# Kernel optimization log

Measured on AMD Instinct MI355X. Metric: run time of the kernel, lower is better.

The kernel has to match this reference:

```python
import jax, jax.numpy as jnp
import numpy as np

N = 100_000      # nodes
E = 1_600_000    # nonzeros of the rescaled Laplacian (avg degree 16)
F_IN = 128
F_OUT = 128
K = 4


def setup_inputs() -> dict:
    key = jax.random.key(0)
    ks = jax.random.split(key, 6)
    x = jax.random.normal(ks[0], (N, F_IN), dtype=jnp.float32)
    filter_coeff = jax.random.normal(ks[1], (K, N), dtype=jnp.float32)
    # glorot-ish scale for [K, F_in, F_out]
    stdv = float(np.sqrt(6.0 / (F_IN + F_OUT)))
    weight = jax.random.uniform(ks[2], (K, F_IN, F_OUT), dtype=jnp.float32,
                                minval=-stdv, maxval=stdv)
    bias = jnp.zeros((F_OUT,), dtype=jnp.float32)
    src = jax.random.randint(ks[3], (E,), 0, N, dtype=jnp.int32)
    dst = jax.random.randint(ks[4], (E,), 0, N, dtype=jnp.int32)
    # edge values of L_hat = 2L/lambda_max - I (precomputed sparse matrix)
    edge_w = jax.random.normal(ks[5], (E,), dtype=jnp.float32) * 0.1
    return {"x": x, "filter_coeff": filter_coeff, "weight": weight,
            "bias": bias, "edge_w": edge_w, "src": src, "dst": dst}


def reference(x, filter_coeff, weight, bias, edge_w, src, dst):
    n = x.shape[0]

    def spmm(h):  # edge-weighted gather-scale-segment_sum == dgl.update_all
        return jax.ops.segment_sum(h[src] * edge_w[:, None], dst,
                                   num_segments=n)

    # Chebyshev recurrence: T0 = x, T1 = L_hat x, T_k = 2 L_hat T_{k-1} - T_{k-2}
    Tx0 = x
    out = (filter_coeff[0][:, None] * Tx0) @ weight[0]
    Tx1 = spmm(x)
    out = out + (filter_coeff[1][:, None] * Tx1) @ weight[1]
    for k in range(2, weight.shape[0]):
        Tx2 = 2.0 * spmm(Tx1) - Tx0
        out = out + (filter_coeff[k][:, None] * Tx2) @ weight[k]
        Tx0, Tx1 = Tx1, Tx2
    return out + bias
```

## Files before the change

kernel.cpp:

```cpp
#include <hip/hip_runtime.h>
#include <hip/hip_bf16.h>
#include <cstdio>

#define F 128
#define BSHIFT 9
#define BROWS 512
#define C2 4096

typedef __attribute__((ext_vector_type(4))) float f32x4;
typedef __attribute__((ext_vector_type(4))) unsigned short u16x4;
typedef __attribute__((ext_vector_type(8))) short s16x8;

__device__ inline unsigned short f2bf(float x) {
  unsigned int u = __float_as_uint(x);
  u += 0x7fffu + ((u >> 16) & 1u);
  return (unsigned short)(u >> 16);
}
__device__ inline float bf2f(unsigned int h) {
  return __uint_as_float(h << 16);
}

__device__ inline void async_load16(const void* g, void* l) {
  __builtin_amdgcn_global_load_lds(
      (const __attribute__((address_space(1))) void*)g,
      (__attribute__((address_space(3))) void*)l, 16, 0, 0);
}

__global__ void bucket_hist_kernel(const int* __restrict__ dst, int* __restrict__ bhist,
                                   int E, int B) {
  __shared__ int h[256];
  int t = threadIdx.x;
  h[t] = 0;
  __syncthreads();
  for (int e = blockIdx.x * blockDim.x + t; e < E; e += gridDim.x * blockDim.x)
    atomicAdd(&h[dst[e] >> BSHIFT], 1);
  __syncthreads();
  if (t < B && h[t]) atomicAdd(&bhist[t], h[t]);
}

__global__ void bucket_scan_kernel(const int* __restrict__ bhist, int* __restrict__ bbase,
                                   int* __restrict__ bcursor, int* __restrict__ rp,
                                   int E, int B, int N) {
  __shared__ int sm[256];
  int t = threadIdx.x;
  int v = (t < B) ? bhist[t] : 0;
  sm[t] = v;
  __syncthreads();
  int x = v;
  for (int off = 1; off < 256; off <<= 1) {
    int add = (t >= off) ? sm[t - off] : 0;
    __syncthreads();
    x += add;
    sm[t] = x;
    __syncthreads();
  }
  int excl = x - v;
  if (t < B) { bbase[t] = excl; bcursor[t] = excl; }
  if (t == 0) { bbase[B] = E; rp[N] = E; }
}

__global__ __launch_bounds__(256) void bucket_scatter_kernel(
    const int* __restrict__ src, const int* __restrict__ dst, const float* __restrict__ ew,
    int* __restrict__ bcursor, unsigned int* __restrict__ stg_p, float* __restrict__ stg_w,
    int E, int B) {
  __shared__ int hist[256], gbase[256], cur[256], sm[256], scn[256];
  __shared__ unsigned int sp[C2];
  __shared__ float swt[C2];
  __shared__ int sdest[C2];
  int t = threadIdx.x;
  int e0 = blockIdx.x * C2;
  int cnt = min(C2, E - e0);
  hist[t] = 0;
  __syncthreads();
#pragma unroll
  for (int i = 0; i < C2 / 256; ++i) {
    int e = e0 + t + i * 256;
    if (e < E) atomicAdd(&hist[dst[e] >> BSHIFT], 1);
  }
  __syncthreads();
  int v = hist[t];
  gbase[t] = (t < B && v) ? atomicAdd(&bcursor[t], v) : 0;
  sm[t] = v;
  __syncthreads();
  int x = v;
  for (int off = 1; off < 256; off <<= 1) {
    int add = (t >= off) ? sm[t - off] : 0;
    __syncthreads();
    x += add;
    sm[t] = x;
    __syncthreads();
  }
  scn[t] = x - v;
  cur[t] = 0;
  __syncthreads();
#pragma unroll
  for (int i = 0; i < C2 / 256; ++i) {
    int e = e0 + t + i * 256;
    if (e < E) {
      int d = dst[e];
      int b = d >> BSHIFT;
      int r = atomicAdd(&cur[b], 1);
      int slot = scn[b] + r;
      sp[slot] = (unsigned int)src[e] | ((unsigned int)(d & (BROWS - 1)) << 17);
      swt[slot] = ew[e];
      sdest[slot] = gbase[b] + r;
    }
  }
  __syncthreads();
#pragma unroll
  for (int i = 0; i < C2 / 256; ++i) {
    int s = t + i * 256;
    if (s < cnt) {
      int dpos = sdest[s];
      stg_p[dpos] = sp[s];
      stg_w[dpos] = swt[s];
    }
  }
}

__global__ __launch_bounds__(256) void csr_build_kernel(
    const unsigned int* __restrict__ stg_p, const float* __restrict__ stg_w,
    const int* __restrict__ bbase, int* __restrict__ rp, int2* __restrict__ csr,
    int N, int B) {
  __shared__ int rhist[BROWS], rloc[BROWS], curp[BROWS];
  __shared__ int sm[256];
  int b = blockIdx.x, t = threadIdx.x;
  int row0 = b << BSHIFT;
  int base = bbase[b];
  int cnt = bbase[b + 1] - base;
  rhist[t] = 0;
  rhist[t + 256] = 0;
  __syncthreads();
  for (int s = base + t; s < base + cnt; s += 256)
    atomicAdd(&rhist[stg_p[s] >> 17], 1);
  __syncthreads();
  int a0 = rhist[2 * t], a1 = rhist[2 * t + 1];
  int pv = a0 + a1;
  sm[t] = pv;
  __syncthreads();
  int x = pv;
  for (int off = 1; off < 256; off <<= 1) {
    int add = (t >= off) ? sm[t - off] : 0;
    __syncthreads();
    x += add;
    sm[t] = x;
    __syncthreads();
  }
  int pexcl = x - pv;
  int r0 = 2 * t, r1 = 2 * t + 1;
  rloc[r0] = pexcl;
  rloc[r1] = pexcl + a0;
  if (row0 + r0 < N) rp[row0 + r0] = base + rloc[r0];
  if (row0 + r1 < N) rp[row0 + r1] = base + rloc[r1];
  curp[r0] = base + rloc[r0];
  curp[r1] = base + rloc[r1];
  __syncthreads();
  for (int s = base + t; s < base + cnt; s += 256) {
    unsigned int p = stg_p[s];
    int dl = p >> 17;
    int pos = atomicAdd(&curp[dl], 1);
    int2 entry;
    entry.x = (int)(p & 0x1ffffu);
    entry.y = __float_as_int(stg_w[s]);
    csr[pos] = entry;
  }
}

__global__ void convx_kernel(const float* __restrict__ x, unsigned short* __restrict__ xbf,
                             int total4) {
  int i = blockIdx.x * 256 + threadIdx.x;
  if (i >= total4) return;
  f32x4 v = ((const f32x4*)x)[i];
  u16x4 o;
  o.x = f2bf(v.x); o.y = f2bf(v.y); o.z = f2bf(v.z); o.w = f2bf(v.w);
  ((u16x4*)xbf)[i] = o;
}

__global__ __launch_bounds__(256) void spmm_kernel(
    const unsigned short* __restrict__ Tin, const unsigned short* __restrict__ Tsub,
    unsigned short* __restrict__ Tout, const int* __restrict__ rp,
    const int2* __restrict__ csr, int n, float scale) {
  int row = blockIdx.x * 16 + (threadIdx.x >> 4);
  if (row >= n) return;
  int sl = threadIdx.x & 15;
  int j0 = rp[row], end = rp[row + 1];
  const uint4* Tin4 = (const uint4*)Tin;
  float acc[8];
#pragma unroll
  for (int c = 0; c < 8; ++c) acc[c] = 0.f;

  for (int j = j0; j < end; j += 8) {
    int2 e[8];
#pragma unroll
    for (int u = 0; u < 8; ++u)
      if (j + u < end) e[u] = csr[j + u];
    uint4 v[8];
#pragma unroll
    for (int u = 0; u < 8; ++u)
      if (j + u < end) v[u] = Tin4[(size_t)e[u].x * 16 + sl];
#pragma unroll
    for (int u = 0; u < 8; ++u) {
      if (j + u < end) {
        float w = __int_as_float(e[u].y);
        acc[0] = fmaf(w, bf2f(v[u].x & 0xffffu), acc[0]);
        acc[1] = fmaf(w, bf2f(v[u].x >> 16), acc[1]);
        acc[2] = fmaf(w, bf2f(v[u].y & 0xffffu), acc[2]);
        acc[3] = fmaf(w, bf2f(v[u].y >> 16), acc[3]);
        acc[4] = fmaf(w, bf2f(v[u].z & 0xffffu), acc[4]);
        acc[5] = fmaf(w, bf2f(v[u].z >> 16), acc[5]);
        acc[6] = fmaf(w, bf2f(v[u].w & 0xffffu), acc[6]);
        acc[7] = fmaf(w, bf2f(v[u].w >> 16), acc[7]);
      }
    }
  }

  float r[8];
#pragma unroll
  for (int c = 0; c < 8; ++c) r[c] = scale * acc[c];
  if (Tsub) {
    uint4 p = ((const uint4*)Tsub)[(size_t)row * 16 + sl];
    r[0] -= bf2f(p.x & 0xffffu); r[1] -= bf2f(p.x >> 16);
    r[2] -= bf2f(p.y & 0xffffu); r[3] -= bf2f(p.y >> 16);
    r[4] -= bf2f(p.z & 0xffffu); r[5] -= bf2f(p.z >> 16);
    r[6] -= bf2f(p.w & 0xffffu); r[7] -= bf2f(p.w >> 16);
  }
  uint4 o;
  o.x = (unsigned)f2bf(r[0]) | ((unsigned)f2bf(r[1]) << 16);
  o.y = (unsigned)f2bf(r[2]) | ((unsigned)f2bf(r[3]) << 16);
  o.z = (unsigned)f2bf(r[4]) | ((unsigned)f2bf(r[5]) << 16);
  o.w = (unsigned)f2bf(r[6]) | ((unsigned)f2bf(r[7]) << 16);
  ((uint4*)Tout)[(size_t)row * 16 + sl] = o;
}

__global__ void convw_kernel(const float* __restrict__ W, unsigned short* __restrict__ Wf,
                             int total) {
  int idx = blockIdx.x * 256 + threadIdx.x;
  if (idx >= total) return;
  int j = idx & 7;
  int lane = (idx >> 3) & 63;
  int nt = (idx >> 9) & 7;
  int kk = (idx >> 12) & 3;
  int ks = idx >> 14;
  int kl = kk * 32 + (lane >> 4) * 8 + j;
  int col = nt * 16 + (lane & 15);
  Wf[idx] = f2bf(W[(size_t)ks * F * F + (size_t)kl * F + col]);
}

struct GemmArgs {
  const unsigned short* A[8];
  const float* fc;
  const unsigned short* Wt;
  const float* bias;
  float* out;
  int n;
  int kslices;
};

__global__ __launch_bounds__(512) void gemm_kernel(GemmArgs args) {
  __shared__ __align__(16) unsigned short SA[16384];
  __shared__ __align__(16) unsigned short SB[16384];
  const int t = threadIdx.x;
  const int lane = t & 63;
  const int wid = t >> 6;
  const int wrow = wid >> 1;
  const int wcol = wid & 1;
  const int n = args.n;
  const int bm = blockIdx.x * 128;
  const int arow = lane & 15;
  const int kg = lane >> 4;

  f32x4 Cf[2][4];
#pragma unroll
  for (int mt = 0; mt < 2; ++mt)
#pragma unroll
    for (int nt = 0; nt < 4; ++nt) Cf[mt][nt] = (f32x4){0.f, 0.f, 0.f, 0.f};

  for (int ks = 0; ks < args.kslices; ++ks) {
    const unsigned short* As = args.A[ks];
#pragma unroll
    for (int i = 0; i < 4; ++i) {
      int fi = wid + i * 8;
      int rg = fi >> 2, kk = fi & 3;
      int r = bm + rg * 16 + arow;
      if (r >= n) r = n - 1;
      const void* g = (const void*)(As + (size_t)r * F + kk * 32 + kg * 8);
      async_load16(g, (void*)(SA + fi * 512));
    }
#pragma unroll
    for (int i = 0; i < 4; ++i) {
      int fi = wid + i * 8;
      const void* g = (const void*)(args.Wt + (size_t)ks * 16384 + fi * 512 + lane * 8);
      async_load16(g, (void*)(SB + fi * 512));
    }
    __syncthreads();

    f32x4 acc[2][4];
#pragma unroll
    for (int mt = 0; mt < 2; ++mt)
#pragma unroll
      for (int nt = 0; nt < 4; ++nt) acc[mt][nt] = (f32x4){0.f, 0.f, 0.f, 0.f};

#pragma unroll
    for (int kk = 0; kk < 4; ++kk) {
      s16x8 af[2], bfr[4];
#pragma unroll
      for (int mt = 0; mt < 2; ++mt) {
        int rg = wrow * 2 + mt;
        af[mt] = *(const s16x8*)&SA[(rg * 4 + kk) * 512 + lane * 8];
      }
#pragma unroll
      for (int nt = 0; nt < 4; ++nt)
        bfr[nt] = *(const s16x8*)&SB[(kk * 8 + wcol * 4 + nt) * 512 + lane * 8];
#pragma unroll
      for (int mt = 0; mt < 2; ++mt)
#pragma unroll
        for (int nt = 0; nt < 4; ++nt)
          acc[mt][nt] = __builtin_amdgcn_mfma_f32_16x16x32_bf16(af[mt], bfr[nt],
                                                                acc[mt][nt], 0, 0, 0);
    }

#pragma unroll
    for (int mt = 0; mt < 2; ++mt) {
      int row = bm + wrow * 32 + mt * 16 + kg * 4;
      f32x4 fv;
      if (row + 3 < n) {
        fv = *(const f32x4*)(args.fc + (size_t)ks * n + row);
      } else {
#pragma unroll
        for (int r4 = 0; r4 < 4; ++r4) {
          int rr = row + r4;
          if (rr >= n) rr = n - 1;
          fv[r4] = args.fc[(size_t)ks * n + rr];
        }
      }
#pragma unroll
      for (int nt = 0; nt < 4; ++nt) Cf[mt][nt] += fv * acc[mt][nt];
    }
    __syncthreads();
  }

#pragma unroll
  for (int nt = 0; nt < 4; ++nt) {
    int col = (wcol * 4 + nt) * 16 + arow;
    float bv = args.bias[col];
#pragma unroll
    for (int mt = 0; mt < 2; ++mt) {
#pragma unroll
      for (int r4 = 0; r4 < 4; ++r4) {
        int row = bm + wrow * 32 + mt * 16 + kg * 4 + r4;
        if (row < n) args.out[(size_t)row * F + col] = Cf[mt][nt][r4] + bv;
      }
    }
  }
}

extern "C" void kernel_launch(void* const* d_in, const int* in_sizes, int n_in,
                              void* d_out, int out_size, void* d_ws, size_t ws_size,
                              hipStream_t stream) {
  const float* x    = (const float*)d_in[0];
  const float* fc   = (const float*)d_in[1];
  const float* W    = (const float*)d_in[2];
  const float* bias = (const float*)d_in[3];
  const float* ew   = (const float*)d_in[4];
  const int*   src  = (const int*)d_in[5];
  const int*   dst  = (const int*)d_in[6];

  const int N = in_sizes[0] / F;
  const int K = in_sizes[2] / (F * F);
  const int E = in_sizes[4];
  const int B = (N + BROWS - 1) >> BSHIFT;

  size_t off = 0;
  char* base = (char*)d_ws;
  auto alloc = [&](size_t bytes) -> void* {
    void* p = base + off;
    off += (bytes + 511) & ~(size_t)511;
    return p;
  };
  int* rp              = (int*)alloc(((size_t)N + 1) * 4);
  int* bhist           = (int*)alloc(1024);
  int* bbase           = (int*)alloc(1040);
  int* bcursor         = (int*)alloc(1024);
  int2* csr            = (int2*)alloc((size_t)E * 8);
  unsigned short* Wt   = (unsigned short*)alloc((size_t)K * F * F * 2);
  unsigned short* xbf  = (unsigned short*)alloc((size_t)N * F * 2);
  unsigned short* T[8];
  T[0] = xbf;
  for (int k = 1; k < K && k < 8; ++k) T[k] = (unsigned short*)alloc((size_t)N * F * 2);
  unsigned int* stg_p;
  float* stg_w;
  if (K >= 3 && (size_t)N * F * 2 >= (size_t)E * 8) {
    stg_p = (unsigned int*)T[2];
    stg_w = (float*)(T[2] + (size_t)E * 2);
  } else {
    stg_p = (unsigned int*)alloc((size_t)E * 4);
    stg_w = (float*)alloc((size_t)E * 4);
  }
  if (off > ws_size) {
    fprintf(stderr, "kernel_launch: ws too small: need %zu have %zu\n", off, ws_size);
    return;
  }

  hipMemsetAsync(bhist, 0, 1024, stream);
  int hblocks = (E + 255) / 256;
  if (hblocks > 2048) hblocks = 2048;
  hipLaunchKernelGGL(bucket_hist_kernel, dim3(hblocks), dim3(256), 0, stream, dst, bhist, E, B);
  hipLaunchKernelGGL(bucket_scan_kernel, dim3(1), dim3(256), 0, stream, bhist, bbase, bcursor,
                     rp, E, B, N);
  int sblocks = (E + C2 - 1) / C2;
  hipLaunchKernelGGL(bucket_scatter_kernel, dim3(sblocks), dim3(256), 0, stream, src, dst, ew,
                     bcursor, stg_p, stg_w, E, B);
  hipLaunchKernelGGL(csr_build_kernel, dim3(B), dim3(256), 0, stream, stg_p, stg_w, bbase,
                     rp, csr, N, B);

  int total4 = N * F / 4;
  hipLaunchKernelGGL(convx_kernel, dim3((total4 + 255) / 256), dim3(256), 0, stream,
                     x, xbf, total4);

  int sb = (N + 15) / 16;
  if (K > 1)
    hipLaunchKernelGGL(spmm_kernel, dim3(sb), dim3(256), 0, stream, xbf,
                       (const unsigned short*)nullptr, T[1], rp, csr, N, 1.0f);
  for (int k = 2; k < K; ++k) {
    const unsigned short* prev = T[k - 2];
    hipLaunchKernelGGL(spmm_kernel, dim3(sb), dim3(256), 0, stream, T[k - 1], prev, T[k],
                       rp, csr, N, 2.0f);
  }

  int total = K * F * F;
  hipLaunchKernelGGL(convw_kernel, dim3((total + 255) / 256), dim3(256), 0, stream, W, Wt,
                     total);

  GemmArgs ga;
  for (int k = 0; k < 8; ++k) ga.A[k] = (k < K) ? T[k] : xbf;
  ga.fc = fc; ga.Wt = Wt; ga.bias = bias;
  ga.out = (float*)d_out;
  ga.n = N; ga.kslices = K;
  hipLaunchKernelGGL(gemm_kernel, dim3((N + 127) / 128), dim3(512), 0, stream, ga);
}
```

Measured before the change: 369.6 us.

## Double-buffer GEMM LDS stages, swap MFMA operands for vectorized output stores

The GEMM now keeps two LDS buffers, so the async global-to-LDS loads for the next K-slice are issued before the current slice is computed, with explicit vmcnt waits and barriers in place of __syncthreads. The MFMA operands are swapped, which transposes the accumulator layout. Each lane then reads one filter coefficient per row tile and writes its output as float4 row stores with a vectorized bias add. The histogram kernel grid is fixed at 208 blocks. LDS use doubles, which may reduce how many blocks fit per CU.

```diff
diff --git a/kernel.cpp b/kernel.cpp
--- a/kernel.cpp
+++ b/kernel.cpp
@@ -257,25 +257,20 @@
 };
 
 __global__ __launch_bounds__(512) void gemm_kernel(GemmArgs args) {
-  __shared__ __align__(16) unsigned short SA[16384];
-  __shared__ __align__(16) unsigned short SB[16384];
+  __shared__ __align__(16) unsigned short SA[2][16384];
+  __shared__ __align__(16) unsigned short SB[2][16384];
   const int t = threadIdx.x;
   const int lane = t & 63;
   const int wid = t >> 6;
   const int wrow = wid >> 1;
   const int wcol = wid & 1;
   const int n = args.n;
+  const int KS = args.kslices;
   const int bm = blockIdx.x * 128;
   const int arow = lane & 15;
   const int kg = lane >> 4;
 
-  f32x4 Cf[2][4];
-#pragma unroll
-  for (int mt = 0; mt < 2; ++mt)
-#pragma unroll
-    for (int nt = 0; nt < 4; ++nt) Cf[mt][nt] = (f32x4){0.f, 0.f, 0.f, 0.f};
-
-  for (int ks = 0; ks < args.kslices; ++ks) {
+  auto stage = [&](int ks, int b) {
     const unsigned short* As = args.A[ks];
 #pragma unroll
     for (int i = 0; i < 4; ++i) {
@@ -283,16 +278,47 @@
       int rg = fi >> 2, kk = fi & 3;
       int r = bm + rg * 16 + arow;
       if (r >= n) r = n - 1;
-      const void* g = (const void*)(As + (size_t)r * F + kk * 32 + kg * 8);
-      async_load16(g, (void*)(SA + fi * 512));
+      async_load16((const void*)(As + (size_t)r * F + kk * 32 + kg * 8),
+                   (void*)(SA[b] + fi * 512));
     }
 #pragma unroll
     for (int i = 0; i < 4; ++i) {
       int fi = wid + i * 8;
-      const void* g = (const void*)(args.Wt + (size_t)ks * 16384 + fi * 512 + lane * 8);
-      async_load16(g, (void*)(SB + fi * 512));
-    }
-    __syncthreads();
+      async_load16((const void*)(args.Wt + (size_t)ks * 16384 + fi * 512 + lane * 8),
+                   (void*)(SB[b] + fi * 512));
+    }
+  };
+
+  f32x4 Cf[2][4];
+#pragma unroll
+  for (int mt = 0; mt < 2; ++mt)
+#pragma unroll
+    for (int nt = 0; nt < 4; ++nt) Cf[mt][nt] = (f32x4){0.f, 0.f, 0.f, 0.f};
+
+  int row_c[2];
+#pragma unroll
+  for (int mt = 0; mt < 2; ++mt) {
+    int r = bm + wrow * 32 + mt * 16 + arow;
+    row_c[mt] = r < n ? r : n - 1;
+  }
+
+  stage(0, 0);
+
+  for (int ks = 0; ks < KS; ++ks) {
+    const int b = ks & 1;
+    if (ks + 1 < KS) {
+      stage(ks + 1, b ^ 1);
+      asm volatile("s_waitcnt vmcnt(8)" ::: "memory");
+    } else {
+      asm volatile("s_waitcnt vmcnt(0)" ::: "memory");
+    }
+    __builtin_amdgcn_sched_barrier(0);
+    __builtin_amdgcn_s_barrier();
+    __builtin_amdgcn_sched_barrier(0);
+
+    float fv[2];
+#pragma unroll
+    for (int mt = 0; mt < 2; ++mt) fv[mt] = args.fc[(size_t)ks * n + row_c[mt]];
 
     f32x4 acc[2][4];
 #pragma unroll
@@ -306,50 +332,38 @@
 #pragma unroll
       for (int mt = 0; mt < 2; ++mt) {
         int rg = wrow * 2 + mt;
-        af[mt] = *(const s16x8*)&SA[(rg * 4 + kk) * 512 + lane * 8];
+        af[mt] = *(const s16x8*)&SA[b][(rg * 4 + kk) * 512 + lane * 8];
       }
 #pragma unroll
       for (int nt = 0; nt < 4; ++nt)
-        bfr[nt] = *(const s16x8*)&SB[(kk * 8 + wcol * 4 + nt) * 512 + lane * 8];
+        bfr[nt] = *(const s16x8*)&SB[b][(kk * 8 + wcol * 4 + nt) * 512 + lane * 8];
 #pragma unroll
       for (int mt = 0; mt < 2; ++mt)
 #pragma unroll
         for (int nt = 0; nt < 4; ++nt)
-          acc[mt][nt] = __builtin_amdgcn_mfma_f32_16x16x32_bf16(af[mt], bfr[nt],
+          acc[mt][nt] = __builtin_amdgcn_mfma_f32_16x16x32_bf16(bfr[nt], af[mt],
                                                                 acc[mt][nt], 0, 0, 0);
     }
 
 #pragma unroll
-    for (int mt = 0; mt < 2; ++mt) {
-      int row = bm + wrow * 32 + mt * 16 + kg * 4;
-      f32x4 fv;
-      if (row + 3 < n) {
-        fv = *(const f32x4*)(args.fc + (size_t)ks * n + row);
-      } else {
-#pragma unroll
-        for (int r4 = 0; r4 < 4; ++r4) {
-          int rr = row + r4;
-          if (rr >= n) rr = n - 1;
-          fv[r4] = args.fc[(size_t)ks * n + rr];
-        }
-      }
-#pragma unroll
-      for (int nt = 0; nt < 4; ++nt) Cf[mt][nt] += fv * acc[mt][nt];
-    }
-    __syncthreads();
-  }
-
-#pragma unroll
-  for (int nt = 0; nt < 4; ++nt) {
-    int col = (wcol * 4 + nt) * 16 + arow;
-    float bv = args.bias[col];
-#pragma unroll
-    for (int mt = 0; mt < 2; ++mt) {
-#pragma unroll
-      for (int r4 = 0; r4 < 4; ++r4) {
-        int row = bm + wrow * 32 + mt * 16 + kg * 4 + r4;
-        if (row < n) args.out[(size_t)row * F + col] = Cf[mt][nt][r4] + bv;
-      }
+    for (int mt = 0; mt < 2; ++mt)
+#pragma unroll
+      for (int nt = 0; nt < 4; ++nt) Cf[mt][nt] += fv[mt] * acc[mt][nt];
+
+    __builtin_amdgcn_sched_barrier(0);
+    __builtin_amdgcn_s_barrier();
+    __builtin_amdgcn_sched_barrier(0);
+  }
+
+#pragma unroll
+  for (int mt = 0; mt < 2; ++mt) {
+    int row = bm + wrow * 32 + mt * 16 + arow;
+    if (row >= n) continue;
+#pragma unroll
+    for (int nt = 0; nt < 4; ++nt) {
+      int col = (wcol * 4 + nt) * 16 + kg * 4;
+      f32x4 bv = *(const f32x4*)(args.bias + col);
+      *(f32x4*)(args.out + (size_t)row * F + col) = Cf[mt][nt] + bv;
     }
   }
 }
@@ -402,9 +416,7 @@
   }
 
   hipMemsetAsync(bhist, 0, 1024, stream);
-  int hblocks = (E + 255) / 256;
-  if (hblocks > 2048) hblocks = 2048;
-  hipLaunchKernelGGL(bucket_hist_kernel, dim3(hblocks), dim3(256), 0, stream, dst, bhist, E, B);
+  hipLaunchKernelGGL(bucket_hist_kernel, dim3(208), dim3(256), 0, stream, dst, bhist, E, B);
   hipLaunchKernelGGL(bucket_scan_kernel, dim3(1), dim3(256), 0, stream, bhist, bbase, bcursor,
                      rp, E, B, N);
   int sblocks = (E + C2 - 1) / C2;
```

Result: faster. 320.3 us (median of 2 runs) (-13.3%).
